# Kernel optimization log

Hardware: AMD Instinct MI355X
Metric: run time of the kernel (lower is better)

Reference implementation:

```python
import jax, jax.numpy as jnp
import numpy as np

B, T, H, D_H, P = 4, 2048, 16, 64, 8
ACTIVE_THRESH = 1e-6


def setup_inputs() -> dict:
    key = jax.random.key(0)
    k1, k2, k3, k4, k5 = jax.random.split(key, 5)
    x_proj = jax.random.normal(k1, (B, T, H, D_H), dtype=jnp.float32)
    proto = 0.02 * jax.random.normal(k2, (P, D_H), dtype=jnp.float32)
    gate = 0.02 * jax.random.normal(k3, (P,), dtype=jnp.float32)
    # nn.Linear default init ~ U(-1/sqrt(fan_in), 1/sqrt(fan_in)); approximate scale
    lim = 1.0 / np.sqrt(D_H)
    w1 = jax.random.uniform(k4, (P, D_H, D_H), minval=-lim, maxval=lim, dtype=jnp.float32)
    w2 = jax.random.uniform(k5, (P, D_H, D_H), minval=-lim, maxval=lim, dtype=jnp.float32)
    return {"x_proj": x_proj, "proto": proto, "gate": gate, "w1": w1, "w2": w2}


def reference(x_proj, proto, gate, w1, w2):
    b, t, h, d_h = x_proj.shape
    p = proto.shape[0]
    # routing logits: [B,T,H,P]
    logits = jnp.einsum('bthd,pd->bthp', x_proj, proto) / jnp.sqrt(jnp.asarray(d_h, x_proj.dtype))
    logits = logits - gate  # broadcast over [P]
    mask = jax.nn.relu(logits)
    mask_flat = mask.reshape(-1, p)  # [S,P]
    # weights: expert contributions zeroed where mask <= 1e-6 (matches torch active_mask gate)
    weight = jnp.where(mask_flat > ACTIVE_THRESH, mask_flat, jnp.zeros_like(mask_flat))
    x_flat = x_proj.reshape(-1, d_h)  # [S,D_h]
    # per-expert 2-layer SiLU MLP, computed densely then masked-combined
    # torch Linear: y = x @ W.T with W [out,in] -> einsum contracts last dim of W
    hmid = jax.nn.silu(jnp.einsum('sd,pod->spo', x_flat, w1))  # [S,P,D_h]
    out = jnp.einsum('spo,pdo->spd', hmid, w2)                 # [S,P,D_h]
    y = jnp.einsum('spd,sp->sd', out, weight)                  # masked scatter-combine
    output = y.reshape(b, t, h, d_h)
    return output, logits, mask
```

## Files before the change

kernel.cpp:

```cpp
#include <hip/hip_runtime.h>
#include <hip/hip_bf16.h>


typedef __attribute__((ext_vector_type(8))) short short8;
typedef __attribute__((ext_vector_type(4))) short bf16x4;
typedef __attribute__((ext_vector_type(4))) float f32x4;
typedef __attribute__((ext_vector_type(4))) unsigned int u32x4;
typedef __attribute__((ext_vector_type(2))) unsigned int u32x2;

#define NEXP 8
#define DH 64
#define BT 256
#define THREADS 512
#define OFF_WT 65536
#define LDS_BYTES (65536 + 8192)

__device__ __forceinline__ unsigned int f2bf(float f) {
    unsigned int u = __builtin_bit_cast(unsigned int, f);
    return (u + 0x7fffu + ((u >> 16) & 1u)) >> 16;
}
__device__ __forceinline__ short bfc(float f) {
    return (short)__bfloat16_as_ushort(__float2bfloat16(f));
}

#if __has_builtin(__builtin_amdgcn_mfma_f32_16x16x16_bf16)
#define MFMA16(a, b, c) __builtin_amdgcn_mfma_f32_16x16x16_bf16(a, b, c, 0, 0, 0)
#else
#define MFMA16(a, b, c) __builtin_amdgcn_mfma_f32_16x16x16bf16_1k(a, b, c, 0, 0, 0)
#endif

typedef const unsigned int __attribute__((address_space(1)))* gas_u32p;
typedef unsigned int __attribute__((address_space(3)))* las_u32p;

__device__ __forceinline__ void glds16(const void* g, void* lbase, int lane) {
#if __has_builtin(__builtin_amdgcn_global_load_lds)
    (void)lane;
    __builtin_amdgcn_global_load_lds((gas_u32p)g, (las_u32p)lbase, 16, 0, 0);
#else
    *reinterpret_cast<u32x4*>(reinterpret_cast<char*>(lbase) + lane * 16) =
        *reinterpret_cast<const u32x4*>(g);
#endif
}

__global__ void prep_w(const float* __restrict__ w1, const float* __restrict__ w2,
                       unsigned char* __restrict__ ws) {
    int q = blockIdx.x * 256 + threadIdx.x;
    int mat = q >> 13;
    int p = (q >> 10) & 7;
    int r = (q >> 4) & 63;
    int dq = q & 15;
    const float* src = (mat ? w2 : w1) + (size_t)(((p << 6) + r) << 6) + (dq << 2);
    f32x4 v = *reinterpret_cast<const f32x4*>(src);
    u32x2 pk;
    pk[0] = f2bf(v[0]) | (f2bf(v[1]) << 16);
    pk[1] = f2bf(v[2]) | (f2bf(v[3]) << 16);
    int col = mat ? (((dq & 3) << 5) | ((dq >> 2) << 3)) : (dq << 3);
    int off = (p << 14) + (mat << 13) + (r << 7) + (col ^ ((r & 7) << 4));
    *reinterpret_cast<u32x2*>(ws + off) = pk;
}

__global__ __launch_bounds__(THREADS, 1)
void spl_main(const float* __restrict__ x, const float* __restrict__ proto,
              const float* __restrict__ gate, const unsigned char* __restrict__ wimg,
              float* __restrict__ y_out, float* __restrict__ logits_out,
              float* __restrict__ mask_out)
{
    extern __shared__ __align__(16) char smem[];
    const int tid = threadIdx.x;
    const int lane = tid & 63;
    const int wv = __builtin_amdgcn_readfirstlane(tid >> 6);
    const int fr = lane & 15;
    const int fg = (lane >> 4) & 3;
    const int sw = (fr & 7) << 4;
    const int t0 = blockIdx.x * BT + wv * 32;

    auto stage = [&](int ps) {
#pragma unroll
        for (int i = 0; i < 8; ++i)
            glds16(wimg + (ps << 16) + i * 8192 + wv * 1024 + lane * 16,
                   smem + i * 8192 + wv * 1024, lane);
    };

    float xv[2][2][8];
#pragma unroll
    for (int n = 0; n < 2; ++n)
#pragma unroll
        for (int kk = 0; kk < 2; ++kk) {
            const float* g = x + (size_t)(t0 + n * 16 + fr) * DH + kk * 32 + fg * 8;
            f32x4 a = *reinterpret_cast<const f32x4*>(g);
            f32x4 b = *reinterpret_cast<const f32x4*>(g + 4);
#pragma unroll
            for (int i = 0; i < 4; ++i) { xv[n][kk][i] = a[i]; xv[n][kk][4 + i] = b[i]; }
        }
    {
        float dot[2][NEXP];
#pragma unroll
        for (int n = 0; n < 2; ++n)
#pragma unroll
            for (int p = 0; p < NEXP; ++p) dot[n][p] = 0.f;
#pragma unroll
        for (int p = 0; p < NEXP; ++p)
#pragma unroll
            for (int kk = 0; kk < 2; ++kk) {
                const float* pr = proto + p * DH + kk * 32 + fg * 8;
                f32x4 p0 = *reinterpret_cast<const f32x4*>(pr);
                f32x4 p1 = *reinterpret_cast<const f32x4*>(pr + 4);
#pragma unroll
                for (int n = 0; n < 2; ++n)
#pragma unroll
                    for (int i = 0; i < 4; ++i)
                        dot[n][p] += xv[n][kk][i] * p0[i] + xv[n][kk][4 + i] * p1[i];
            }
        float lg[2][NEXP], mk[2][NEXP];
#pragma unroll
        for (int n = 0; n < 2; ++n)
#pragma unroll
            for (int p = 0; p < NEXP; ++p) {
                float v = dot[n][p];
                v += __shfl_xor(v, 16);
                v += __shfl_xor(v, 32);
                lg[n][p] = v * 0.125f - gate[p];
                mk[n][p] = fmaxf(lg[n][p], 0.f);
            }
        int ns = fg & 1;
        size_t rowb = (size_t)(t0 + ns * 16 + fr) * NEXP;
        f32x4 v0, v1;
        if (fg < 2) {
#pragma unroll
            for (int i = 0; i < 4; ++i) { v0[i] = lg[ns][i]; v1[i] = lg[ns][4 + i]; }
            *reinterpret_cast<f32x4*>(logits_out + rowb) = v0;
            *reinterpret_cast<f32x4*>(logits_out + rowb + 4) = v1;
        } else {
#pragma unroll
            for (int i = 0; i < 4; ++i) { v0[i] = mk[ns][i]; v1[i] = mk[ns][4 + i]; }
            *reinterpret_cast<f32x4*>(mask_out + rowb) = v0;
            *reinterpret_cast<f32x4*>(mask_out + rowb + 4) = v1;
            f32x4 w0, w1v;
#pragma unroll
            for (int i = 0; i < 4; ++i) {
                w0[i]  = (v0[i] > 1e-6f) ? v0[i] : 0.f;
                w1v[i] = (v1[i] > 1e-6f) ? v1[i] : 0.f;
            }
            char* wb = smem + OFF_WT + (wv * 32 + ns * 16 + fr) * 32;
            *reinterpret_cast<f32x4*>(wb) = w0;
            *reinterpret_cast<f32x4*>(wb + 16) = w1v;
        }
    }

    stage(0);

    short8 xb[2][2];
#pragma unroll
    for (int n = 0; n < 2; ++n)
#pragma unroll
        for (int kk = 0; kk < 2; ++kk) {
            short8 t;
#pragma unroll
            for (int j = 0; j < 8; ++j) t[j] = bfc(xv[n][kk][j]);
            xb[n][kk] = t;
        }
    __syncthreads();

    f32x4 yacc[4][2];
#pragma unroll
    for (int mt = 0; mt < 4; ++mt)
#pragma unroll
        for (int n = 0; n < 2; ++n) yacc[mt][n] = (f32x4){0.f, 0.f, 0.f, 0.f};

    const float* const wtp = reinterpret_cast<const float*>(smem + OFF_WT);

#pragma unroll 1
    for (int ps = 0; ps < 2; ++ps) {
        if (ps) {
            __syncthreads();
            stage(1);
            __syncthreads();
        }
#pragma unroll 1
        for (int q = 0; q < 4; ++q) {
            const int p = ps * 4 + q;
            const char* sW1 = smem + (q << 14);
            const char* sW2 = sW1 + 8192;
            const float wt0 = wtp[(wv * 32 + fr) * 8 + p];
            const float wt1 = wtp[(wv * 32 + 16 + fr) * 8 + p];

#pragma unroll
            for (int h = 0; h < 2; ++h) {
                short8 w1f[2][2];
#pragma unroll
                for (int mtl = 0; mtl < 2; ++mtl)
#pragma unroll
                    for (int kk = 0; kk < 2; ++kk)
                        w1f[mtl][kk] = *reinterpret_cast<const short8*>(
                            sW1 + (h * 32 + mtl * 16 + fr) * 128 +
                            ((kk * 64 + fg * 16) ^ sw));
                f32x4 acc1[2][2];
#pragma unroll
                for (int mtl = 0; mtl < 2; ++mtl)
#pragma unroll
                    for (int n = 0; n < 2; ++n) acc1[mtl][n] = (f32x4){0.f, 0.f, 0.f, 0.f};
#pragma unroll
                for (int kk = 0; kk < 2; ++kk)
#pragma unroll
                    for (int mtl = 0; mtl < 2; ++mtl)
#pragma unroll
                        for (int n = 0; n < 2; ++n)
                            acc1[mtl][n] = __builtin_amdgcn_mfma_f32_16x16x32_bf16(
                                w1f[mtl][kk], xb[n][kk], acc1[mtl][n], 0, 0, 0);

                bf16x4 pkB[2][2];
#pragma unroll
                for (int mtl = 0; mtl < 2; ++mtl)
#pragma unroll
                    for (int n = 0; n < 2; ++n) {
                        const float wt = n ? wt1 : wt0;
                        bf16x4 t;
#pragma unroll
                        for (int r = 0; r < 4; ++r) {
                            float hd = acc1[mtl][n][r];
                            float s = hd * __builtin_amdgcn_rcpf(1.f + __expf(-hd));
                            t[r] = bfc(wt * s);
                        }
                        pkB[mtl][n] = t;
                    }

#pragma unroll
                for (int mt = 0; mt < 4; ++mt) {
                    u32x4 wq = *reinterpret_cast<const u32x4*>(
                        sW2 + (mt * 16 + fr) * 128 + ((fg * 32 + h * 16) ^ sw));
                    u32x2 lo2 = {wq[0], wq[1]}, hi2 = {wq[2], wq[3]};
                    bf16x4 wlo = __builtin_bit_cast(bf16x4, lo2);
                    bf16x4 whi = __builtin_bit_cast(bf16x4, hi2);
#pragma unroll
                    for (int n = 0; n < 2; ++n) {
                        yacc[mt][n] = MFMA16(wlo, pkB[0][n], yacc[mt][n]);
                        yacc[mt][n] = MFMA16(whi, pkB[1][n], yacc[mt][n]);
                    }
                }
            }
        }
    }

    __syncthreads();
    char* const yb = smem + wv * 8192;
#pragma unroll
    for (int mt = 0; mt < 4; ++mt)
#pragma unroll
        for (int n = 0; n < 2; ++n) {
            f32x4 v;
#pragma unroll
            for (int r = 0; r < 4; ++r) v[r] = yacc[mt][n][r];
            *reinterpret_cast<f32x4*>(
                yb + (n * 16 + fr) * 256 + ((mt * 64 + fg * 16) ^ sw)) = v;
        }
    __builtin_amdgcn_s_waitcnt(0);
#pragma unroll
    for (int it = 0; it < 8; ++it) {
        const int r = it * 4 + (lane >> 4);
        const int cb = (lane & 15) * 16;
        f32x4 v = *reinterpret_cast<const f32x4*>(yb + r * 256 + (cb ^ ((r & 7) << 4)));
        *reinterpret_cast<f32x4*>(
            reinterpret_cast<char*>(y_out) + (size_t)(t0 + r) * 256 + cb) = v;
    }
}

extern "C" void kernel_launch(void* const* d_in, const int* in_sizes, int n_in,
                              void* d_out, int out_size, void* d_ws, size_t ws_size,
                              hipStream_t stream) {
    (void)n_in; (void)out_size; (void)ws_size;
    const float* x     = (const float*)d_in[0];
    const float* proto = (const float*)d_in[1];
    const float* gate  = (const float*)d_in[2];
    const float* w1    = (const float*)d_in[3];
    const float* w2    = (const float*)d_in[4];
    float* y = (float*)d_out;
    const int S = in_sizes[0] / DH;
    float* logits = y + (size_t)S * DH;
    float* mask   = logits + (size_t)S * NEXP;
    unsigned char* wimg = (unsigned char*)d_ws;

    prep_w<<<64, 256, 0, stream>>>(w1, w2, wimg);
    (void)hipFuncSetAttribute(reinterpret_cast<const void*>(spl_main),
                              hipFuncAttributeMaxDynamicSharedMemorySize, LDS_BYTES);
    spl_main<<<S / BT, THREADS, LDS_BYTES, stream>>>(x, proto, gate, wimg,
                                                     y, logits, mask);
}
```

Measured before the change: 55.16 us.

## Halve threads per block and give each wave 64 tokens for weight-fragment reuse

Each block drops from 8 waves to 4, and each wave now handles 64 tokens instead of 32. Every W1/W2 fragment loaded from LDS therefore feeds twice as many MFMAs, and the routing softmax work is spread so that every lane writes logits and mask. The per-expert gate weights are stored in LDS laid out by expert, and LDS addresses are precomputed. In exchange, per-wave register use roughly doubles (accumulators and x fragments), and fewer waves per CU are left to hide latency.

```diff
diff --git a/kernel.cpp b/kernel.cpp
--- a/kernel.cpp
+++ b/kernel.cpp
@@ -11,7 +11,7 @@
 #define NEXP 8
 #define DH 64
 #define BT 256
-#define THREADS 512
+#define THREADS 256
 #define OFF_WT 65536
 #define LDS_BYTES (65536 + 8192)
 
@@ -72,18 +72,19 @@
     const int fr = lane & 15;
     const int fg = (lane >> 4) & 3;
     const int sw = (fr & 7) << 4;
-    const int t0 = blockIdx.x * BT + wv * 32;
+    const int t0 = blockIdx.x * BT + wv * 64;
 
     auto stage = [&](int ps) {
 #pragma unroll
-        for (int i = 0; i < 8; ++i)
-            glds16(wimg + (ps << 16) + i * 8192 + wv * 1024 + lane * 16,
-                   smem + i * 8192 + wv * 1024, lane);
+        for (int i = 0; i < 16; ++i) {
+            const int ch = (i * 4 + wv) << 10;
+            glds16(wimg + (ps << 16) + ch + lane * 16, smem + ch, lane);
+        }
     };
 
-    float xv[2][2][8];
-#pragma unroll
-    for (int n = 0; n < 2; ++n)
+    float xv[4][2][8];
+#pragma unroll
+    for (int n = 0; n < 4; ++n)
 #pragma unroll
         for (int kk = 0; kk < 2; ++kk) {
             const float* g = x + (size_t)(t0 + n * 16 + fr) * DH + kk * 32 + fg * 8;
@@ -93,9 +94,9 @@
             for (int i = 0; i < 4; ++i) { xv[n][kk][i] = a[i]; xv[n][kk][4 + i] = b[i]; }
         }
     {
-        float dot[2][NEXP];
-#pragma unroll
-        for (int n = 0; n < 2; ++n)
+        float dot[4][NEXP];
+#pragma unroll
+        for (int n = 0; n < 4; ++n)
 #pragma unroll
             for (int p = 0; p < NEXP; ++p) dot[n][p] = 0.f;
 #pragma unroll
@@ -106,52 +107,46 @@
                 f32x4 p0 = *reinterpret_cast<const f32x4*>(pr);
                 f32x4 p1 = *reinterpret_cast<const f32x4*>(pr + 4);
 #pragma unroll
-                for (int n = 0; n < 2; ++n)
+                for (int n = 0; n < 4; ++n)
 #pragma unroll
                     for (int i = 0; i < 4; ++i)
                         dot[n][p] += xv[n][kk][i] * p0[i] + xv[n][kk][4 + i] * p1[i];
             }
-        float lg[2][NEXP], mk[2][NEXP];
-#pragma unroll
-        for (int n = 0; n < 2; ++n)
-#pragma unroll
-            for (int p = 0; p < NEXP; ++p) {
-                float v = dot[n][p];
-                v += __shfl_xor(v, 16);
-                v += __shfl_xor(v, 32);
-                lg[n][p] = v * 0.125f - gate[p];
-                mk[n][p] = fmaxf(lg[n][p], 0.f);
-            }
-        int ns = fg & 1;
-        size_t rowb = (size_t)(t0 + ns * 16 + fr) * NEXP;
+        float lgs[NEXP], mks[NEXP];
+#pragma unroll
+        for (int p = 0; p < NEXP; ++p) {
+            float s0 = dot[0][p], s1 = dot[1][p], s2 = dot[2][p], s3 = dot[3][p];
+            s0 += __shfl_xor(s0, 16); s0 += __shfl_xor(s0, 32);
+            s1 += __shfl_xor(s1, 16); s1 += __shfl_xor(s1, 32);
+            s2 += __shfl_xor(s2, 16); s2 += __shfl_xor(s2, 32);
+            s3 += __shfl_xor(s3, 16); s3 += __shfl_xor(s3, 32);
+            float sel = (fg & 2) ? ((fg & 1) ? s3 : s2) : ((fg & 1) ? s1 : s0);
+            float l = sel * 0.125f - gate[p];
+            lgs[p] = l;
+            mks[p] = fmaxf(l, 0.f);
+        }
+        size_t rowb = (size_t)(t0 + fg * 16 + fr) * NEXP;
         f32x4 v0, v1;
-        if (fg < 2) {
-#pragma unroll
-            for (int i = 0; i < 4; ++i) { v0[i] = lg[ns][i]; v1[i] = lg[ns][4 + i]; }
-            *reinterpret_cast<f32x4*>(logits_out + rowb) = v0;
-            *reinterpret_cast<f32x4*>(logits_out + rowb + 4) = v1;
-        } else {
-#pragma unroll
-            for (int i = 0; i < 4; ++i) { v0[i] = mk[ns][i]; v1[i] = mk[ns][4 + i]; }
-            *reinterpret_cast<f32x4*>(mask_out + rowb) = v0;
-            *reinterpret_cast<f32x4*>(mask_out + rowb + 4) = v1;
-            f32x4 w0, w1v;
-#pragma unroll
-            for (int i = 0; i < 4; ++i) {
-                w0[i]  = (v0[i] > 1e-6f) ? v0[i] : 0.f;
-                w1v[i] = (v1[i] > 1e-6f) ? v1[i] : 0.f;
-            }
-            char* wb = smem + OFF_WT + (wv * 32 + ns * 16 + fr) * 32;
-            *reinterpret_cast<f32x4*>(wb) = w0;
-            *reinterpret_cast<f32x4*>(wb + 16) = w1v;
+#pragma unroll
+        for (int i = 0; i < 4; ++i) { v0[i] = lgs[i]; v1[i] = lgs[4 + i]; }
+        *reinterpret_cast<f32x4*>(logits_out + rowb) = v0;
+        *reinterpret_cast<f32x4*>(logits_out + rowb + 4) = v1;
+#pragma unroll
+        for (int i = 0; i < 4; ++i) { v0[i] = mks[i]; v1[i] = mks[4 + i]; }
+        *reinterpret_cast<f32x4*>(mask_out + rowb) = v0;
+        *reinterpret_cast<f32x4*>(mask_out + rowb + 4) = v1;
+#pragma unroll
+        for (int p = 0; p < NEXP; ++p) {
+            float w = (mks[p] > 1e-6f) ? mks[p] : 0.f;
+            *reinterpret_cast<float*>(
+                smem + OFF_WT + (p << 10) + (wv * 64 + fg * 16 + fr) * 4) = w;
         }
     }
 
     stage(0);
-
-    short8 xb[2][2];
-#pragma unroll
-    for (int n = 0; n < 2; ++n)
+    short8 xb[4][2];
+#pragma unroll
+    for (int n = 0; n < 4; ++n)
 #pragma unroll
         for (int kk = 0; kk < 2; ++kk) {
             short8 t;
@@ -161,92 +156,91 @@
         }
     __syncthreads();
 
-    f32x4 yacc[4][2];
+    f32x4 yacc[4][4];
 #pragma unroll
     for (int mt = 0; mt < 4; ++mt)
 #pragma unroll
-        for (int n = 0; n < 2; ++n) yacc[mt][n] = (f32x4){0.f, 0.f, 0.f, 0.f};
-
-    const float* const wtp = reinterpret_cast<const float*>(smem + OFF_WT);
+        for (int n = 0; n < 4; ++n) yacc[mt][n] = (f32x4){0.f, 0.f, 0.f, 0.f};
+
+    const int aW1k0 = fr * 128 + ((fg * 16) ^ sw);
+    const int aW1k1 = fr * 128 + ((64 + fg * 16) ^ sw);
+    const int aW2h0 = 8192 + fr * 128 + ((fg * 32) ^ sw);
+    const int aW2h1 = 8192 + fr * 128 + ((16 + fg * 32) ^ sw);
+    const int awt = OFF_WT + (wv * 64 + fr) * 4;
 
 #pragma unroll 1
-    for (int ps = 0; ps < 2; ++ps) {
-        if (ps) {
+    for (int p = 0; p < NEXP; ++p) {
+        if (p == 4) {
             __syncthreads();
             stage(1);
             __syncthreads();
         }
-#pragma unroll 1
-        for (int q = 0; q < 4; ++q) {
-            const int p = ps * 4 + q;
-            const char* sW1 = smem + (q << 14);
-            const char* sW2 = sW1 + 8192;
-            const float wt0 = wtp[(wv * 32 + fr) * 8 + p];
-            const float wt1 = wtp[(wv * 32 + 16 + fr) * 8 + p];
-
-#pragma unroll
-            for (int h = 0; h < 2; ++h) {
-                short8 w1f[2][2];
+        char* const eb = smem + ((p & 3) << 14);
+        float wtn[4];
+#pragma unroll
+        for (int n = 0; n < 4; ++n)
+            wtn[n] = *reinterpret_cast<const float*>(smem + awt - OFF_WT + OFF_WT +
+                                                     (p << 10) + n * 64);
+#pragma unroll
+        for (int h = 0; h < 2; ++h) {
+            short8 w1f[2][2];
+#pragma unroll
+            for (int mtl = 0; mtl < 2; ++mtl) {
+                const int ro = (h * 32 + mtl * 16) * 128;
+                w1f[mtl][0] = *reinterpret_cast<const short8*>(eb + aW1k0 + ro);
+                w1f[mtl][1] = *reinterpret_cast<const short8*>(eb + aW1k1 + ro);
+            }
+            f32x4 acc1[2][4];
+#pragma unroll
+            for (int mtl = 0; mtl < 2; ++mtl)
+#pragma unroll
+                for (int n = 0; n < 4; ++n) acc1[mtl][n] = (f32x4){0.f, 0.f, 0.f, 0.f};
+#pragma unroll
+            for (int kk = 0; kk < 2; ++kk)
 #pragma unroll
                 for (int mtl = 0; mtl < 2; ++mtl)
 #pragma unroll
-                    for (int kk = 0; kk < 2; ++kk)
-                        w1f[mtl][kk] = *reinterpret_cast<const short8*>(
-                            sW1 + (h * 32 + mtl * 16 + fr) * 128 +
-                            ((kk * 64 + fg * 16) ^ sw));
-                f32x4 acc1[2][2];
-#pragma unroll
-                for (int mtl = 0; mtl < 2; ++mtl)
-#pragma unroll
-                    for (int n = 0; n < 2; ++n) acc1[mtl][n] = (f32x4){0.f, 0.f, 0.f, 0.f};
-#pragma unroll
-                for (int kk = 0; kk < 2; ++kk)
-#pragma unroll
-                    for (int mtl = 0; mtl < 2; ++mtl)
-#pragma unroll
-                        for (int n = 0; n < 2; ++n)
-                            acc1[mtl][n] = __builtin_amdgcn_mfma_f32_16x16x32_bf16(
-                                w1f[mtl][kk], xb[n][kk], acc1[mtl][n], 0, 0, 0);
-
-                bf16x4 pkB[2][2];
-#pragma unroll
-                for (int mtl = 0; mtl < 2; ++mtl)
-#pragma unroll
-                    for (int n = 0; n < 2; ++n) {
-                        const float wt = n ? wt1 : wt0;
-                        bf16x4 t;
-#pragma unroll
-                        for (int r = 0; r < 4; ++r) {
-                            float hd = acc1[mtl][n][r];
-                            float s = hd * __builtin_amdgcn_rcpf(1.f + __expf(-hd));
-                            t[r] = bfc(wt * s);
-                        }
-                        pkB[mtl][n] = t;
+                    for (int n = 0; n < 4; ++n)
+                        acc1[mtl][n] = __builtin_amdgcn_mfma_f32_16x16x32_bf16(
+                            w1f[mtl][kk], xb[n][kk], acc1[mtl][n], 0, 0, 0);
+
+            bf16x4 pkB[2][4];
+#pragma unroll
+            for (int mtl = 0; mtl < 2; ++mtl)
+#pragma unroll
+                for (int n = 0; n < 4; ++n) {
+                    bf16x4 t;
+#pragma unroll
+                    for (int r = 0; r < 4; ++r) {
+                        float hd = acc1[mtl][n][r];
+                        float s = hd * __builtin_amdgcn_rcpf(1.f + __expf(-hd));
+                        t[r] = bfc(wtn[n] * s);
                     }
-
-#pragma unroll
-                for (int mt = 0; mt < 4; ++mt) {
-                    u32x4 wq = *reinterpret_cast<const u32x4*>(
-                        sW2 + (mt * 16 + fr) * 128 + ((fg * 32 + h * 16) ^ sw));
-                    u32x2 lo2 = {wq[0], wq[1]}, hi2 = {wq[2], wq[3]};
-                    bf16x4 wlo = __builtin_bit_cast(bf16x4, lo2);
-                    bf16x4 whi = __builtin_bit_cast(bf16x4, hi2);
-#pragma unroll
-                    for (int n = 0; n < 2; ++n) {
-                        yacc[mt][n] = MFMA16(wlo, pkB[0][n], yacc[mt][n]);
-                        yacc[mt][n] = MFMA16(whi, pkB[1][n], yacc[mt][n]);
-                    }
+                    pkB[mtl][n] = t;
+                }
+
+            const int aW2 = h ? aW2h1 : aW2h0;
+#pragma unroll
+            for (int mt = 0; mt < 4; ++mt) {
+                u32x4 wq = *reinterpret_cast<const u32x4*>(eb + aW2 + mt * 16 * 128);
+                u32x2 lo2 = {wq[0], wq[1]}, hi2 = {wq[2], wq[3]};
+                bf16x4 wlo = __builtin_bit_cast(bf16x4, lo2);
+                bf16x4 whi = __builtin_bit_cast(bf16x4, hi2);
+#pragma unroll
+                for (int n = 0; n < 4; ++n) {
+                    yacc[mt][n] = MFMA16(wlo, pkB[0][n], yacc[mt][n]);
+                    yacc[mt][n] = MFMA16(whi, pkB[1][n], yacc[mt][n]);
                 }
             }
         }
     }
 
     __syncthreads();
-    char* const yb = smem + wv * 8192;
+    char* const yb = smem + wv * 16384;
 #pragma unroll
     for (int mt = 0; mt < 4; ++mt)
 #pragma unroll
-        for (int n = 0; n < 2; ++n) {
+        for (int n = 0; n < 4; ++n) {
             f32x4 v;
 #pragma unroll
             for (int r = 0; r < 4; ++r) v[r] = yacc[mt][n][r];
@@ -255,7 +249,7 @@
         }
     __builtin_amdgcn_s_waitcnt(0);
 #pragma unroll
-    for (int it = 0; it < 8; ++it) {
+    for (int it = 0; it < 16; ++it) {
         const int r = it * 4 + (lane >> 4);
         const int cb = (lane & 15) * 16;
         f32x4 v = *reinterpret_cast<const f32x4*>(yb + r * 256 + (cb ^ ((r & 7) << 4)));
```

Result: slower. 64.39 us (+16.7%).
